# Kernel optimization log

Hardware: AMD Instinct MI355X
Metric: run time of the kernel (lower is better)

The kernel has to match this reference:

```python
import jax, jax.numpy as jnp
import numpy as np


def setup_inputs() -> dict:
    key = jax.random.key(0)
    k1, k2 = jax.random.split(key)
    context_emb = jax.random.normal(k1, (8, 2048, 768), dtype=jnp.float32)
    query_emb = jax.random.normal(k2, (8, 512, 768), dtype=jnp.float32)
    return {"context_emb": context_emb, "query_emb": query_emb}


def reference(context_emb, query_emb):
    # temp[b, q, c] = sum_d query[b,q,d] * context[b,c,d]
    temp = jnp.einsum("bqd,bcd->bqc", query_emb, context_emb)
    # softmax over the query axis (dim=1 in torch)
    alpha = jax.nn.softmax(temp, axis=1)  # [B, Lq, Lc]
    # attention_weighted_query[b, c, d] = sum_q query[b,q,d] * alpha[b,q,c]
    awq = jnp.einsum("bqd,bqc->bcd", query_emb, alpha)  # [B, Lc, D]
    # elementwise gate against context
    return context_emb * awq
```

## Files before the change

kernel.cpp:

```cpp
#include <hip/hip_runtime.h>
#include <hip/hip_bf16.h>

#define NB 8
#define LQ 512
#define LC 2048
#define DD 768

typedef _Float16 f16x8 __attribute__((ext_vector_type(8)));
typedef _Float16 f16x4 __attribute__((ext_vector_type(4)));
typedef float    f32x4 __attribute__((ext_vector_type(4)));

__global__ __launch_bounds__(256) void convert_ctx(const float* __restrict__ src,
                                                   _Float16* __restrict__ dst) {
    const size_t i = (size_t)blockIdx.x * 256 + threadIdx.x;
    const f32x4* s = (const f32x4*)src;
    f32x4 a = s[i * 2 + 0];
    f32x4 b = s[i * 2 + 1];
    f16x8 h;
    h[0] = (_Float16)a.x; h[1] = (_Float16)a.y; h[2] = (_Float16)a.z; h[3] = (_Float16)a.w;
    h[4] = (_Float16)b.x; h[5] = (_Float16)b.y; h[6] = (_Float16)b.z; h[7] = (_Float16)b.w;
    ((f16x8*)dst)[i] = h;
}

__global__ __launch_bounds__(256) void preconvert_q(const float* __restrict__ Q,
                                                    _Float16* __restrict__ Qh,
                                                    _Float16* __restrict__ QhT) {
    __shared__ _Float16 lt[64][68];
    const int blk = blockIdx.x;
    const int b   = blk / 96;
    const int rem = blk % 96;
    const int q0  = (rem / 12) * 64;
    const int d0  = (rem % 12) * 64;
    const int t   = threadIdx.x;
    const int tr  = t >> 4;
    const int tc  = t & 15;

    const float* Qb  = Q  + ((size_t)b * LQ + q0) * DD + d0;
    _Float16*    Qhb = Qh + ((size_t)b * LQ + q0) * DD + d0;

#pragma unroll
    for (int i = 0; i < 4; i++) {
        const int row = i * 16 + tr;
        const int col = tc * 4;
        f32x4 v = *(const f32x4*)(Qb + (size_t)row * DD + col);
        f16x4 h;
        h.x = (_Float16)v.x; h.y = (_Float16)v.y;
        h.z = (_Float16)v.z; h.w = (_Float16)v.w;
        *(f16x4*)(Qhb + (size_t)row * DD + col) = h;
        *(f16x4*)&lt[row][col] = h;
    }
    __syncthreads();

    _Float16* QTb = QhT + ((size_t)b * DD + d0) * LQ + q0;
#pragma unroll
    for (int i = 0; i < 4; i++) {
        const int drow = i * 16 + tr;
        const int qc   = tc * 4;
        f16x4 h;
        h.x = lt[qc + 0][drow];
        h.y = lt[qc + 1][drow];
        h.z = lt[qc + 2][drow];
        h.w = lt[qc + 3][drow];
        *(f16x4*)(QTb + (size_t)drow * LQ + qc) = h;
    }
}

#define LDSA_STRIDE 776
#define PSTRIDE     520
#define BBUF0_OFF   49664
#define CBUF0_OFF   33280
#define CBUF1_OFF   82432
#define RED_OFF     131584
#define SMEM_BYTES  133632

template <bool USE_CH>
__global__ __launch_bounds__(512, 2) void gated_attn(const float* __restrict__ ctx,
                                                     const _Float16* __restrict__ Ch,
                                                     const _Float16* __restrict__ Qh,
                                                     const _Float16* __restrict__ QhT,
                                                     float* __restrict__ out) {
    __shared__ __align__(16) char smem[SMEM_BYTES];
    _Float16* ldsA = (_Float16*)smem;
    _Float16* ldsP = (_Float16*)smem;
    float (*red_max)[32] = (float (*)[32])(smem + RED_OFF);
    float (*red_sum)[32] = (float (*)[32])(smem + RED_OFF + 1024);

    const int b    = blockIdx.x & 7;
    const int c0   = (blockIdx.x >> 3) * 32;
    const int t    = threadIdx.x;
    const int w    = t >> 6;
    const int lane = t & 63;
    const int quad = lane >> 4;
    const int l15  = lane & 15;
    const int srow = t >> 2;
    const int ssub = t & 3;

    const float*    Cb  = ctx + ((size_t)b * LC + c0) * DD;
    const _Float16* Chb = USE_CH ? (Ch + ((size_t)b * LC + c0) * DD) : nullptr;
    const _Float16* Qhb = Qh  + (size_t)b * LQ * DD;
    const _Float16* QTb = QhT + (size_t)b * DD * LQ;

#pragma unroll
    for (int i = 0; i < 6; i++) {
        const int idx  = i * 512 + t;
        const int row  = idx / 96;
        const int colc = idx % 96;
        f16x8 v;
        if (USE_CH) {
            v = *(const f16x8*)(Chb + (size_t)row * DD + colc * 8);
        } else {
            const float* p = Cb + (size_t)row * DD + colc * 8;
            f32x4 f0 = *(const f32x4*)p;
            f32x4 f1 = *(const f32x4*)(p + 4);
            v[0] = (_Float16)f0.x; v[1] = (_Float16)f0.y;
            v[2] = (_Float16)f0.z; v[3] = (_Float16)f0.w;
            v[4] = (_Float16)f1.x; v[5] = (_Float16)f1.y;
            v[6] = (_Float16)f1.z; v[7] = (_Float16)f1.w;
        }
        *(f16x8*)&ldsA[row * LDSA_STRIDE + colc * 8] = v;
    }

    f16x8 sb[4];
#pragma unroll
    for (int j = 0; j < 4; j++)
        sb[j] = *(const f16x8*)(Qhb + (size_t)(j * 128 + srow) * DD + ssub * 8);
    {
        _Float16* bw = (_Float16*)(smem + BBUF0_OFF);
#pragma unroll
        for (int j = 0; j < 4; j++)
            *(f16x8*)&bw[(j * 128 + srow) * 32 + ssub * 8] = sb[j];
    }
    __syncthreads();

    f32x4 acc[2][4];
#pragma unroll
    for (int mt = 0; mt < 2; mt++)
#pragma unroll
        for (int nt = 0; nt < 4; nt++)
            acc[mt][nt] = (f32x4){0.f, 0.f, 0.f, 0.f};

#pragma unroll
    for (int kc = 0; kc < 24; kc++) {
        if (kc + 1 < 24) {
#pragma unroll
            for (int j = 0; j < 4; j++)
                sb[j] = *(const f16x8*)(Qhb + (size_t)(j * 128 + srow) * DD + (kc + 1) * 32 + ssub * 8);
        }
        if (kc > 0) __syncthreads();
        const _Float16* bbuf = (const _Float16*)(smem + BBUF0_OFF + (kc & 1) * 32768);
        f16x8 a0 = *(const f16x8*)&ldsA[(size_t)l15        * LDSA_STRIDE + kc * 32 + quad * 8];
        f16x8 a1 = *(const f16x8*)&ldsA[(size_t)(16 + l15) * LDSA_STRIDE + kc * 32 + quad * 8];
#pragma unroll
        for (int nt = 0; nt < 4; nt++) {
            f16x8 bq = *(const f16x8*)&bbuf[(w * 64 + nt * 16 + l15) * 32 + quad * 8];
            acc[0][nt] = __builtin_amdgcn_mfma_f32_16x16x32_f16(a0, bq, acc[0][nt], 0, 0, 0);
            acc[1][nt] = __builtin_amdgcn_mfma_f32_16x16x32_f16(a1, bq, acc[1][nt], 0, 0, 0);
        }
        if (kc + 1 < 24) {
            _Float16* bw = (_Float16*)(smem + BBUF0_OFF + ((kc + 1) & 1) * 32768);
#pragma unroll
            for (int j = 0; j < 4; j++)
                *(f16x8*)&bw[(j * 128 + srow) * 32 + ssub * 8] = sb[j];
        }
    }

    f16x8 sc[6];
#pragma unroll
    for (int j = 0; j < 6; j++)
        sc[j] = *(const f16x8*)(QTb + (size_t)(j * 128 + srow) * LQ + ssub * 8);

    float rm[2][4];
#pragma unroll
    for (int mt = 0; mt < 2; mt++)
#pragma unroll
        for (int r = 0; r < 4; r++)
            rm[mt][r] = -1e30f;
#pragma unroll
    for (int mt = 0; mt < 2; mt++)
#pragma unroll
        for (int nt = 0; nt < 4; nt++) {
            rm[mt][0] = fmaxf(rm[mt][0], acc[mt][nt].x);
            rm[mt][1] = fmaxf(rm[mt][1], acc[mt][nt].y);
            rm[mt][2] = fmaxf(rm[mt][2], acc[mt][nt].z);
            rm[mt][3] = fmaxf(rm[mt][3], acc[mt][nt].w);
        }
#pragma unroll
    for (int off = 1; off < 16; off <<= 1)
#pragma unroll
        for (int mt = 0; mt < 2; mt++)
#pragma unroll
            for (int r = 0; r < 4; r++)
                rm[mt][r] = fmaxf(rm[mt][r], __shfl_xor(rm[mt][r], off));
    if (l15 == 0) {
#pragma unroll
        for (int mt = 0; mt < 2; mt++)
#pragma unroll
            for (int r = 0; r < 4; r++)
                red_max[w][mt * 16 + quad * 4 + r] = rm[mt][r];
    }
    __syncthreads();

    {
        _Float16* cw = (_Float16*)(smem + CBUF0_OFF);
#pragma unroll
        for (int j = 0; j < 6; j++)
            *(f16x8*)&cw[(j * 128 + srow) * 32 + ssub * 8] = sc[j];
    }

    float fm[2][4];
#pragma unroll
    for (int mt = 0; mt < 2; mt++)
#pragma unroll
        for (int r = 0; r < 4; r++) {
            const int row = mt * 16 + quad * 4 + r;
            float m0 = fmaxf(fmaxf(red_max[0][row], red_max[1][row]),
                             fmaxf(red_max[2][row], red_max[3][row]));
            float m1 = fmaxf(fmaxf(red_max[4][row], red_max[5][row]),
                             fmaxf(red_max[6][row], red_max[7][row]));
            fm[mt][r] = fmaxf(m0, m1);
        }
    float rs[2][4];
#pragma unroll
    for (int mt = 0; mt < 2; mt++)
#pragma unroll
        for (int r = 0; r < 4; r++)
            rs[mt][r] = 0.f;
#pragma unroll
    for (int mt = 0; mt < 2; mt++)
#pragma unroll
        for (int nt = 0; nt < 4; nt++) {
            float e0 = __expf(acc[mt][nt].x - fm[mt][0]);
            float e1 = __expf(acc[mt][nt].y - fm[mt][1]);
            float e2 = __expf(acc[mt][nt].z - fm[mt][2]);
            float e3 = __expf(acc[mt][nt].w - fm[mt][3]);
            acc[mt][nt].x = e0; acc[mt][nt].y = e1;
            acc[mt][nt].z = e2; acc[mt][nt].w = e3;
            rs[mt][0] += e0; rs[mt][1] += e1; rs[mt][2] += e2; rs[mt][3] += e3;
        }
#pragma unroll
    for (int off = 1; off < 16; off <<= 1)
#pragma unroll
        for (int mt = 0; mt < 2; mt++)
#pragma unroll
            for (int r = 0; r < 4; r++)
                rs[mt][r] += __shfl_xor(rs[mt][r], off);
    if (l15 == 0) {
#pragma unroll
        for (int mt = 0; mt < 2; mt++)
#pragma unroll
            for (int r = 0; r < 4; r++)
                red_sum[w][mt * 16 + quad * 4 + r] = rs[mt][r];
    }
    __syncthreads();
#pragma unroll
    for (int mt = 0; mt < 2; mt++)
#pragma unroll
        for (int r = 0; r < 4; r++) {
            const int row = mt * 16 + quad * 4 + r;
            float s = 0.f;
#pragma unroll
            for (int j = 0; j < 8; j++) s += red_sum[j][row];
            const float inv = 1.0f / s;
#pragma unroll
            for (int nt = 0; nt < 4; nt++) {
                const int q = w * 64 + nt * 16 + l15;
                float v = (r == 0 ? acc[mt][nt].x : r == 1 ? acc[mt][nt].y
                          : r == 2 ? acc[mt][nt].z : acc[mt][nt].w);
                ldsP[row * PSTRIDE + q] = (_Float16)(v * inv);
            }
        }
    __syncthreads();

    f32x4 acc2[2][6];
#pragma unroll
    for (int mt = 0; mt < 2; mt++)
#pragma unroll
        for (int nt = 0; nt < 6; nt++)
            acc2[mt][nt] = (f32x4){0.f, 0.f, 0.f, 0.f};

#pragma unroll
    for (int kc = 0; kc < 16; kc++) {
        if (kc + 1 < 16) {
#pragma unroll
            for (int j = 0; j < 6; j++)
                sc[j] = *(const f16x8*)(QTb + (size_t)(j * 128 + srow) * LQ + (kc + 1) * 32 + ssub * 8);
        }
        if (kc > 0) __syncthreads();
        const _Float16* cbuf = (const _Float16*)(smem + ((kc & 1) ? CBUF1_OFF : CBUF0_OFF));
        f16x8 a0 = *(const f16x8*)&ldsP[(size_t)l15        * PSTRIDE + kc * 32 + quad * 8];
        f16x8 a1 = *(const f16x8*)&ldsP[(size_t)(16 + l15) * PSTRIDE + kc * 32 + quad * 8];
#pragma unroll
        for (int nt = 0; nt < 6; nt++) {
            f16x8 cq = *(const f16x8*)&cbuf[(w * 96 + nt * 16 + l15) * 32 + quad * 8];
            acc2[0][nt] = __builtin_amdgcn_mfma_f32_16x16x32_f16(a0, cq, acc2[0][nt], 0, 0, 0);
            acc2[1][nt] = __builtin_amdgcn_mfma_f32_16x16x32_f16(a1, cq, acc2[1][nt], 0, 0, 0);
        }
        if (kc + 1 < 16) {
            _Float16* cw = (_Float16*)(smem + (((kc + 1) & 1) ? CBUF1_OFF : CBUF0_OFF));
#pragma unroll
            for (int j = 0; j < 6; j++)
                *(f16x8*)&cw[(j * 128 + srow) * 32 + ssub * 8] = sc[j];
        }
    }

#pragma unroll
    for (int mt = 0; mt < 2; mt++)
#pragma unroll
        for (int nt = 0; nt < 6; nt++) {
            const int col = w * 96 + nt * 16 + l15;
#pragma unroll
            for (int r = 0; r < 4; r++) {
                const int rl  = mt * 16 + quad * 4 + r;
                const int row = c0 + rl;
                const size_t idx = ((size_t)b * LC + row) * DD + col;
                float v = (r == 0 ? acc2[mt][nt].x : r == 1 ? acc2[mt][nt].y
                          : r == 2 ? acc2[mt][nt].z : acc2[mt][nt].w);
                float g = USE_CH ? (float)Chb[(size_t)rl * DD + col] : ctx[idx];
                out[idx] = g * v;
            }
        }
}

extern "C" void kernel_launch(void* const* d_in, const int* in_sizes, int n_in,
                              void* d_out, int out_size, void* d_ws, size_t ws_size,
                              hipStream_t stream) {
    const float* ctx = (const float*)d_in[0];
    const float* q   = (const float*)d_in[1];
    float* out = (float*)d_out;

    const size_t nQ = (size_t)NB * LQ * DD;
    const size_t nC = (size_t)NB * LC * DD;
    _Float16* Qh  = (_Float16*)d_ws;
    _Float16* QhT = Qh + nQ;
    _Float16* Ch  = QhT + nQ;
    const bool use_ch = ws_size >= (2 * nQ + nC) * sizeof(_Float16);

    preconvert_q<<<dim3(NB * 96), dim3(256), 0, stream>>>(q, Qh, QhT);
    if (use_ch) {
        convert_ctx<<<dim3((int)(nC / (256 * 8))), dim3(256), 0, stream>>>(ctx, Ch);
        gated_attn<true><<<dim3(NB * (LC / 32)), dim3(512), 0, stream>>>(ctx, Ch, Qh, QhT, out);
    } else {
        gated_attn<false><<<dim3(NB * (LC / 32)), dim3(512), 0, stream>>>(ctx, nullptr, Qh, QhT, out);
    }
}
```

Baseline: 181.7 us.

## Load Q operands directly from global into MFMA registers, drop LDS staging and ctx preconvert

```diff
diff --git a/kernel.cpp b/kernel.cpp
--- a/kernel.cpp
+++ b/kernel.cpp
@@ -1,5 +1,4 @@
 #include <hip/hip_runtime.h>
-#include <hip/hip_bf16.h>
 
 #define NB 8
 #define LQ 512
@@ -9,18 +8,6 @@
 typedef _Float16 f16x8 __attribute__((ext_vector_type(8)));
 typedef _Float16 f16x4 __attribute__((ext_vector_type(4)));
 typedef float    f32x4 __attribute__((ext_vector_type(4)));
-
-__global__ __launch_bounds__(256) void convert_ctx(const float* __restrict__ src,
-                                                   _Float16* __restrict__ dst) {
-    const size_t i = (size_t)blockIdx.x * 256 + threadIdx.x;
-    const f32x4* s = (const f32x4*)src;
-    f32x4 a = s[i * 2 + 0];
-    f32x4 b = s[i * 2 + 1];
-    f16x8 h;
-    h[0] = (_Float16)a.x; h[1] = (_Float16)a.y; h[2] = (_Float16)a.z; h[3] = (_Float16)a.w;
-    h[4] = (_Float16)b.x; h[5] = (_Float16)b.y; h[6] = (_Float16)b.z; h[7] = (_Float16)b.w;
-    ((f16x8*)dst)[i] = h;
-}
 
 __global__ __launch_bounds__(256) void preconvert_q(const float* __restrict__ Q,
                                                     _Float16* __restrict__ Qh,
@@ -67,15 +54,10 @@
 
 #define LDSA_STRIDE 776
 #define PSTRIDE     520
-#define BBUF0_OFF   49664
-#define CBUF0_OFF   33280
-#define CBUF1_OFF   82432
-#define RED_OFF     131584
-#define SMEM_BYTES  133632
-
-template <bool USE_CH>
-__global__ __launch_bounds__(512, 2) void gated_attn(const float* __restrict__ ctx,
-                                                     const _Float16* __restrict__ Ch,
+#define RED_OFF     49664
+#define SMEM_BYTES  51712
+
+__global__ __launch_bounds__(512, 4) void gated_attn(const float* __restrict__ ctx,
                                                      const _Float16* __restrict__ Qh,
                                                      const _Float16* __restrict__ QhT,
                                                      float* __restrict__ out) {
@@ -92,11 +74,8 @@
     const int lane = t & 63;
     const int quad = lane >> 4;
     const int l15  = lane & 15;
-    const int srow = t >> 2;
-    const int ssub = t & 3;
 
     const float*    Cb  = ctx + ((size_t)b * LC + c0) * DD;
-    const _Float16* Chb = USE_CH ? (Ch + ((size_t)b * LC + c0) * DD) : nullptr;
     const _Float16* Qhb = Qh  + (size_t)b * LQ * DD;
     const _Float16* QTb = QhT + (size_t)b * DD * LQ;
 
@@ -105,30 +84,15 @@
         const int idx  = i * 512 + t;
         const int row  = idx / 96;
         const int colc = idx % 96;
+        const float* p = Cb + (size_t)row * DD + colc * 8;
+        f32x4 f0 = *(const f32x4*)p;
+        f32x4 f1 = *(const f32x4*)(p + 4);
         f16x8 v;
-        if (USE_CH) {
-            v = *(const f16x8*)(Chb + (size_t)row * DD + colc * 8);
-        } else {
-            const float* p = Cb + (size_t)row * DD + colc * 8;
-            f32x4 f0 = *(const f32x4*)p;
-            f32x4 f1 = *(const f32x4*)(p + 4);
-            v[0] = (_Float16)f0.x; v[1] = (_Float16)f0.y;
-            v[2] = (_Float16)f0.z; v[3] = (_Float16)f0.w;
-            v[4] = (_Float16)f1.x; v[5] = (_Float16)f1.y;
-            v[6] = (_Float16)f1.z; v[7] = (_Float16)f1.w;
-        }
+        v[0] = (_Float16)f0.x; v[1] = (_Float16)f0.y;
+        v[2] = (_Float16)f0.z; v[3] = (_Float16)f0.w;
+        v[4] = (_Float16)f1.x; v[5] = (_Float16)f1.y;
+        v[6] = (_Float16)f1.z; v[7] = (_Float16)f1.w;
         *(f16x8*)&ldsA[row * LDSA_STRIDE + colc * 8] = v;
-    }
-
-    f16x8 sb[4];
-#pragma unroll
-    for (int j = 0; j < 4; j++)
-        sb[j] = *(const f16x8*)(Qhb + (size_t)(j * 128 + srow) * DD + ssub * 8);
-    {
-        _Float16* bw = (_Float16*)(smem + BBUF0_OFF);
-#pragma unroll
-        for (int j = 0; j < 4; j++)
-            *(f16x8*)&bw[(j * 128 + srow) * 32 + ssub * 8] = sb[j];
     }
     __syncthreads();
 
@@ -139,35 +103,18 @@
         for (int nt = 0; nt < 4; nt++)
             acc[mt][nt] = (f32x4){0.f, 0.f, 0.f, 0.f};
 
+    const _Float16* bqb = Qhb + (size_t)(w * 64 + l15) * DD + quad * 8;
 #pragma unroll
     for (int kc = 0; kc < 24; kc++) {
-        if (kc + 1 < 24) {
-#pragma unroll
-            for (int j = 0; j < 4; j++)
-                sb[j] = *(const f16x8*)(Qhb + (size_t)(j * 128 + srow) * DD + (kc + 1) * 32 + ssub * 8);
-        }
-        if (kc > 0) __syncthreads();
-        const _Float16* bbuf = (const _Float16*)(smem + BBUF0_OFF + (kc & 1) * 32768);
         f16x8 a0 = *(const f16x8*)&ldsA[(size_t)l15        * LDSA_STRIDE + kc * 32 + quad * 8];
         f16x8 a1 = *(const f16x8*)&ldsA[(size_t)(16 + l15) * LDSA_STRIDE + kc * 32 + quad * 8];
 #pragma unroll
         for (int nt = 0; nt < 4; nt++) {
-            f16x8 bq = *(const f16x8*)&bbuf[(w * 64 + nt * 16 + l15) * 32 + quad * 8];
+            f16x8 bq = *(const f16x8*)(bqb + (size_t)(nt * 16) * DD + kc * 32);
             acc[0][nt] = __builtin_amdgcn_mfma_f32_16x16x32_f16(a0, bq, acc[0][nt], 0, 0, 0);
             acc[1][nt] = __builtin_amdgcn_mfma_f32_16x16x32_f16(a1, bq, acc[1][nt], 0, 0, 0);
         }
-        if (kc + 1 < 24) {
-            _Float16* bw = (_Float16*)(smem + BBUF0_OFF + ((kc + 1) & 1) * 32768);
-#pragma unroll
-            for (int j = 0; j < 4; j++)
-                *(f16x8*)&bw[(j * 128 + srow) * 32 + ssub * 8] = sb[j];
-        }
-    }
-
-    f16x8 sc[6];
-#pragma unroll
-    for (int j = 0; j < 6; j++)
-        sc[j] = *(const f16x8*)(QTb + (size_t)(j * 128 + srow) * LQ + ssub * 8);
+    }
 
     float rm[2][4];
 #pragma unroll
@@ -199,13 +146,6 @@
                 red_max[w][mt * 16 + quad * 4 + r] = rm[mt][r];
     }
     __syncthreads();
-
-    {
-        _Float16* cw = (_Float16*)(smem + CBUF0_OFF);
-#pragma unroll
-        for (int j = 0; j < 6; j++)
-            *(f16x8*)&cw[(j * 128 + srow) * 32 + ssub * 8] = sc[j];
-    }
 
     float fm[2][4];
 #pragma unroll
@@ -252,6 +192,7 @@
                 red_sum[w][mt * 16 + quad * 4 + r] = rs[mt][r];
     }
     __syncthreads();
+
 #pragma unroll
     for (int mt = 0; mt < 2; mt++)
 #pragma unroll
@@ -278,28 +219,16 @@
         for (int nt = 0; nt < 6; nt++)
             acc2[mt][nt] = (f32x4){0.f, 0.f, 0.f, 0.f};
 
+    const _Float16* cqb = QTb + (size_t)(w * 96 + l15) * LQ + quad * 8;
 #pragma unroll
     for (int kc = 0; kc < 16; kc++) {
-        if (kc + 1 < 16) {
-#pragma unroll
-            for (int j = 0; j < 6; j++)
-                sc[j] = *(const f16x8*)(QTb + (size_t)(j * 128 + srow) * LQ + (kc + 1) * 32 + ssub * 8);
-        }
-        if (kc > 0) __syncthreads();
-        const _Float16* cbuf = (const _Float16*)(smem + ((kc & 1) ? CBUF1_OFF : CBUF0_OFF));
         f16x8 a0 = *(const f16x8*)&ldsP[(size_t)l15        * PSTRIDE + kc * 32 + quad * 8];
         f16x8 a1 = *(const f16x8*)&ldsP[(size_t)(16 + l15) * PSTRIDE + kc * 32 + quad * 8];
 #pragma unroll
         for (int nt = 0; nt < 6; nt++) {
-            f16x8 cq = *(const f16x8*)&cbuf[(w * 96 + nt * 16 + l15) * 32 + quad * 8];
+            f16x8 cq = *(const f16x8*)(cqb + (size_t)(nt * 16) * LQ + kc * 32);
             acc2[0][nt] = __builtin_amdgcn_mfma_f32_16x16x32_f16(a0, cq, acc2[0][nt], 0, 0, 0);
             acc2[1][nt] = __builtin_amdgcn_mfma_f32_16x16x32_f16(a1, cq, acc2[1][nt], 0, 0, 0);
-        }
-        if (kc + 1 < 16) {
-            _Float16* cw = (_Float16*)(smem + (((kc + 1) & 1) ? CBUF1_OFF : CBUF0_OFF));
-#pragma unroll
-            for (int j = 0; j < 6; j++)
-                *(f16x8*)&cw[(j * 128 + srow) * 32 + ssub * 8] = sc[j];
         }
     }
 
@@ -315,8 +244,7 @@
                 const size_t idx = ((size_t)b * LC + row) * DD + col;
                 float v = (r == 0 ? acc2[mt][nt].x : r == 1 ? acc2[mt][nt].y
                           : r == 2 ? acc2[mt][nt].z : acc2[mt][nt].w);
-                float g = USE_CH ? (float)Chb[(size_t)rl * DD + col] : ctx[idx];
-                out[idx] = g * v;
+                out[idx] = ctx[idx] * v;
             }
         }
 }
@@ -329,17 +257,9 @@
     float* out = (float*)d_out;
 
     const size_t nQ = (size_t)NB * LQ * DD;
-    const size_t nC = (size_t)NB * LC * DD;
     _Float16* Qh  = (_Float16*)d_ws;
     _Float16* QhT = Qh + nQ;
-    _Float16* Ch  = QhT + nQ;
-    const bool use_ch = ws_size >= (2 * nQ + nC) * sizeof(_Float16);
 
     preconvert_q<<<dim3(NB * 96), dim3(256), 0, stream>>>(q, Qh, QhT);
-    if (use_ch) {
-        convert_ctx<<<dim3((int)(nC / (256 * 8))), dim3(256), 0, stream>>>(ctx, Ch);
-        gated_attn<true><<<dim3(NB * (LC / 32)), dim3(512), 0, stream>>>(ctx, Ch, Qh, QhT, out);
-    } else {
-        gated_attn<false><<<dim3(NB * (LC / 32)), dim3(512), 0, stream>>>(ctx, nullptr, Qh, QhT, out);
-    }
+    gated_attn<<<dim3(NB * (LC / 32)), dim3(512), 0, stream>>>(ctx, Qh, QhT, out);
 }
```

After: 205.7 us. 13.2% more time.
